# Performance work log

Hardware: AMD Instinct MI355X
Metric: run time of the kernel (lower is better)

## Reference

```python
import jax, jax.numpy as jnp
import numpy as np

N_NODES = 50000
N_EDGES = 800000


def gcn_conv(x, W, b, src, dst, n):
    """PyG-style GCNConv: add self-loops, symmetric deg normalization,
    out[i] = sum_{j->i} deg[i]^-1/2 deg[j]^-1/2 (x @ W)[j] + b."""
    h = x @ W                                   # [n, d_out]
    loop = jnp.arange(n, dtype=src.dtype)
    s = jnp.concatenate([src, loop])            # sources incl self-loops
    d = jnp.concatenate([dst, loop])            # destinations incl self-loops
    deg = jax.ops.segment_sum(jnp.ones_like(d, dtype=h.dtype), d, num_segments=n)
    dinv = jax.lax.rsqrt(jnp.maximum(deg, 1.0))
    norm = dinv[s] * dinv[d]                    # [E+n]
    msg = norm[:, None] * h[s]                  # gather + scale, [E+n, d_out]
    out = jax.ops.segment_sum(msg, d, num_segments=n)  # scatter-add
    return out + b


def setup_inputs() -> dict:
    key = jax.random.key(0)
    ks = jax.random.split(key, 8)
    x = jax.random.normal(ks[0], (N_NODES, 128), dtype=jnp.float32)
    edge_index = jax.random.randint(ks[1], (2, N_EDGES), 0, N_NODES, dtype=jnp.int64)
    def glorot(k, shape):
        lim = np.sqrt(6.0 / (shape[0] + shape[1])).astype(np.float32)
        return jax.random.uniform(k, shape, dtype=jnp.float32, minval=-lim, maxval=lim)
    return {
        "x": x,
        "edge_index": edge_index,
        "W1": glorot(ks[2], (128, 128)), "b1": jnp.zeros((128,), jnp.float32),
        "W2": glorot(ks[3], (128, 64)),  "b2": jnp.zeros((64,), jnp.float32),
        "W3": glorot(ks[4], (64, 16)),   "b3": jnp.zeros((16,), jnp.float32),
    }


def reference(x, edge_index, W1, b1, W2, b2, W3, b3):
    src, dst = edge_index[0], edge_index[1]
    n = x.shape[0]
    # base_model: 2-layer GCN
    h = gcn_conv(x, W1, b1, src, dst, n)
    h = jax.nn.relu(h)
    h = gcn_conv(h, W2, b2, src, dst, n)
    # added layer + softmax over class dim
    logits = gcn_conv(h, W3, b3, src, dst, n)
    return jax.nn.softmax(logits, axis=1)
```

## Files before the change

### kernel.cpp

```cpp
#include <hip/hip_runtime.h>
#include <hip/hip_fp16.h>

#define CAP 64


template<int DIN, int DOUT, int TM, int TN, int KC, int EPB>
__global__ __launch_bounds__(256) void k_fused1(const float* __restrict__ X,
                                                const float* __restrict__ W,
                                                __half* __restrict__ Y, int n, int G_scat,
                                                const int* __restrict__ src,
                                                const int* __restrict__ dst,
                                                int* __restrict__ cnt,
                                                unsigned short* __restrict__ srcS, int E) {
    constexpr int CG = DOUT / TN;
    constexpr int RG = 256 / CG;
    constexpr int TILE_R = RG * TM;
    constexpr int NCHUNK = DIN / KC;
    constexpr int XS = KC + 4;
    __shared__ float wsh[KC * DOUT];
    __shared__ float xs[TILE_R * XS];

    if (blockIdx.x < G_scat) {
        int base = blockIdx.x * 256 * EPB + threadIdx.x;
#pragma unroll
        for (int k = 0; k < EPB; ++k) {
            int e = base + k * 256;
            if (e < E) {
                int d = dst[e];
                int pos = atomicAdd(&cnt[d], 1);
                if (pos < CAP) srcS[(size_t)d * CAP + pos] = (unsigned short)src[e];
            }
        }
        return;
    }

    const int rb = (blockIdx.x - G_scat) * TILE_R;
    const int cg = threadIdx.x % CG;
    const int rg = threadIdx.x / CG;
    const int c0 = cg * TN;
    const int r0 = rg * TM;

    float acc[TM][TN] = {};

    for (int kc = 0; kc < NCHUNK; ++kc) {
        const int k0 = kc * KC;
        const float4* wg = reinterpret_cast<const float4*>(W + (size_t)k0 * DOUT);
        for (int i = threadIdx.x; i < KC * DOUT / 4; i += 256)
            reinterpret_cast<float4*>(wsh)[i] = wg[i];
        for (int i = threadIdx.x; i < TILE_R * KC / 4; i += 256) {
            int r = i / (KC / 4);
            int kk = (i % (KC / 4)) * 4;
            int row = rb + r;
            float4 v = {0.f, 0.f, 0.f, 0.f};
            if (row < n) v = *reinterpret_cast<const float4*>(X + (size_t)row * DIN + k0 + kk);
            *reinterpret_cast<float4*>(&xs[r * XS + kk]) = v;
        }
        __syncthreads();
#pragma unroll 4
        for (int k = 0; k < KC; ++k) {
            float wr[TN], xr[TM];
#pragma unroll
            for (int j = 0; j < TN; j += 4)
                *reinterpret_cast<float4*>(&wr[j]) =
                    *reinterpret_cast<const float4*>(&wsh[k * DOUT + c0 + j]);
#pragma unroll
            for (int i = 0; i < TM; ++i) xr[i] = xs[(r0 + i) * XS + k];
#pragma unroll
            for (int i = 0; i < TM; ++i)
#pragma unroll
                for (int j = 0; j < TN; ++j)
                    acc[i][j] = fmaf(xr[i], wr[j], acc[i][j]);
        }
        __syncthreads();
    }

#pragma unroll
    for (int i = 0; i < TM; ++i) {
        int row = rb + r0 + i;
        if (row < n) {
            union { float4 f4; __half h[8]; } u;
#pragma unroll
            for (int j = 0; j < TN; ++j) u.h[j] = __float2half_rn(acc[i][j]);
            *reinterpret_cast<float4*>(Y + (size_t)row * DOUT + c0) = u.f4;
        }
    }
}


__global__ __launch_bounds__(256) void k_g1_gemm2(const __half* __restrict__ t1,
                                                  const int* __restrict__ cnt,
                                                  const unsigned short* __restrict__ srcS,
                                                  const float* __restrict__ b1,
                                                  const float* __restrict__ W2,
                                                  __half* __restrict__ t2, int n) {
    __shared__ float h_sh[32][132];
    const int rb = blockIdx.x * 32;
    const int tid = threadIdx.x;
    const int c = tid & 15;
    const int gl = tid >> 4;

    for (int pass = 0; pass < 2; ++pass) {
        const int lrow = pass * 16 + gl;
        const int i = rb + lrow;
        if (i < n) {
            const int ci = cnt[i];
            const float di = rsqrtf((float)ci + 1.0f);
            float acc[8];
            float4 v = reinterpret_cast<const float4*>(t1)[(size_t)i * 16 + c];
            const __half2* hp = reinterpret_cast<const __half2*>(&v);
#pragma unroll
            for (int q = 0; q < 4; ++q) {
                float2 f = __half22float2(hp[q]);
                acc[2 * q] = di * f.x; acc[2 * q + 1] = di * f.y;
            }
            const int e1 = min(ci, CAP);
            const unsigned short* sp = srcS + (size_t)i * CAP;
#pragma unroll 4
            for (int e = 0; e < e1; ++e) {
                int s = sp[e];
                float ds = rsqrtf((float)cnt[s] + 1.0f);
                float4 w = reinterpret_cast<const float4*>(t1)[(size_t)s * 16 + c];
                const __half2* wp = reinterpret_cast<const __half2*>(&w);
#pragma unroll
                for (int q = 0; q < 4; ++q) {
                    float2 f = __half22float2(wp[q]);
                    acc[2 * q]     = fmaf(ds, f.x, acc[2 * q]);
                    acc[2 * q + 1] = fmaf(ds, f.y, acc[2 * q + 1]);
                }
            }
#pragma unroll
            for (int q = 0; q < 8; ++q) {
                float r = fmaf(di, acc[q], b1[c * 8 + q]);
                h_sh[lrow][c * 8 + q] = fmaxf(r, 0.f);
            }
        } else {
#pragma unroll
            for (int q = 0; q < 8; ++q) h_sh[lrow][c * 8 + q] = 0.f;
        }
    }
    __syncthreads();

    const int c0 = (tid & 15) * 4;
    const int r0 = (tid >> 4) * 2;
    float facc[2][4] = {};
#pragma unroll 8
    for (int k = 0; k < 128; ++k) {
        float4 wr = *reinterpret_cast<const float4*>(W2 + (size_t)k * 64 + c0);
        float x0 = h_sh[r0][k];
        float x1 = h_sh[r0 + 1][k];
        facc[0][0] = fmaf(x0, wr.x, facc[0][0]); facc[0][1] = fmaf(x0, wr.y, facc[0][1]);
        facc[0][2] = fmaf(x0, wr.z, facc[0][2]); facc[0][3] = fmaf(x0, wr.w, facc[0][3]);
        facc[1][0] = fmaf(x1, wr.x, facc[1][0]); facc[1][1] = fmaf(x1, wr.y, facc[1][1]);
        facc[1][2] = fmaf(x1, wr.z, facc[1][2]); facc[1][3] = fmaf(x1, wr.w, facc[1][3]);
    }
#pragma unroll
    for (int i = 0; i < 2; ++i) {
        int row = rb + r0 + i;
        if (row < n) {
            float di = rsqrtf((float)cnt[row] + 1.0f);
            union { float2 f2; __half h[4]; } u;
#pragma unroll
            for (int j = 0; j < 4; ++j) u.h[j] = __float2half_rn(di * facc[i][j]);
            *reinterpret_cast<float2*>(t2 + (size_t)row * 64 + c0) = u.f2;
        }
    }
}


__global__ __launch_bounds__(256) void k_g2_gemm3(const __half* __restrict__ t2,
                                                  const int* __restrict__ cnt,
                                                  const unsigned short* __restrict__ srcS,
                                                  const float* __restrict__ b2,
                                                  const float* __restrict__ W3,
                                                  __half* __restrict__ t3, int n) {
    __shared__ float h_sh[32][68];
    __shared__ float wsh[64 * 16];
    const int rb = blockIdx.x * 32;
    const int tid = threadIdx.x;
    const int c = tid & 7;
    const int g = tid >> 3;
    const int i = rb + g;
    if (i < n) {
        const int ci = cnt[i];
        const float di = rsqrtf((float)ci + 1.0f);
        float acc[8];
        float4 v = reinterpret_cast<const float4*>(t2)[(size_t)i * 8 + c];
        const __half2* hp = reinterpret_cast<const __half2*>(&v);
#pragma unroll
        for (int q = 0; q < 4; ++q) {
            float2 f = __half22float2(hp[q]);
            acc[2 * q] = f.x; acc[2 * q + 1] = f.y;
        }
        const int e1 = min(ci, CAP);
        const unsigned short* sp = srcS + (size_t)i * CAP;
#pragma unroll 4
        for (int e = 0; e < e1; ++e) {
            int s = sp[e];
            float4 w = reinterpret_cast<const float4*>(t2)[(size_t)s * 8 + c];
            const __half2* wp = reinterpret_cast<const __half2*>(&w);
#pragma unroll
            for (int q = 0; q < 4; ++q) {
                float2 f = __half22float2(wp[q]);
                acc[2 * q] += f.x; acc[2 * q + 1] += f.y;
            }
        }
#pragma unroll
        for (int q = 0; q < 8; ++q)
            h_sh[g][c * 8 + q] = fmaf(di, acc[q], b2[c * 8 + q]);
    } else {
#pragma unroll
        for (int q = 0; q < 8; ++q) h_sh[g][c * 8 + q] = 0.f;
    }
    __syncthreads();
    reinterpret_cast<float4*>(wsh)[tid] = reinterpret_cast<const float4*>(W3)[tid];
    __syncthreads();

    const int row = tid >> 3;
    const int col2 = (tid & 7) * 2;
    float a0 = 0.f, a1 = 0.f;
#pragma unroll 8
    for (int k = 0; k < 64; ++k) {
        float x = h_sh[row][k];
        a0 = fmaf(x, wsh[k * 16 + col2], a0);
        a1 = fmaf(x, wsh[k * 16 + col2 + 1], a1);
    }
    int grow = rb + row;
    if (grow < n) {
        float di = rsqrtf((float)cnt[grow] + 1.0f);
        union { unsigned int u32; __half h[2]; } u;
        u.h[0] = __float2half_rn(di * a0);
        u.h[1] = __float2half_rn(di * a1);
        *reinterpret_cast<unsigned int*>(t3 + (size_t)grow * 16 + col2) = u.u32;
    }
}


__global__ __launch_bounds__(256) void k_g3_softmax(const __half* __restrict__ t3,
                                                    const int* __restrict__ cnt,
                                                    const unsigned short* __restrict__ srcS,
                                                    const float* __restrict__ b3,
                                                    float* __restrict__ out, int n) {
    int tid = blockIdx.x * 256 + threadIdx.x;
    int i = tid >> 1;
    if (i >= n) return;
    int c = tid & 1;
    const float4* t4 = reinterpret_cast<const float4*>(t3);
    float acc[8];
    {
        float4 v = t4[(size_t)i * 2 + c];
        const __half2* hp = reinterpret_cast<const __half2*>(&v);
#pragma unroll
        for (int q = 0; q < 4; ++q) {
            float2 f = __half22float2(hp[q]);
            acc[2 * q] = f.x; acc[2 * q + 1] = f.y;
        }
    }
    const int ci = cnt[i];
    const float di = rsqrtf((float)ci + 1.0f);
    const int e1 = min(ci, CAP);
    const unsigned short* sp = srcS + (size_t)i * CAP;
#pragma unroll 4
    for (int e = 0; e < e1; ++e) {
        int s = sp[e];
        float4 v = t4[(size_t)s * 2 + c];
        const __half2* hp = reinterpret_cast<const __half2*>(&v);
#pragma unroll
        for (int q = 0; q < 4; ++q) {
            float2 f = __half22float2(hp[q]);
            acc[2 * q] += f.x; acc[2 * q + 1] += f.y;
        }
    }
    float r[8];
    const float* bp = b3 + c * 8;
#pragma unroll
    for (int q = 0; q < 8; ++q) r[q] = fmaf(di, acc[q], bp[q]);
    float m = r[0];
#pragma unroll
    for (int q = 1; q < 8; ++q) m = fmaxf(m, r[q]);
    m = fmaxf(m, __shfl_xor(m, 1, 2));
    float s = 0.f;
#pragma unroll
    for (int q = 0; q < 8; ++q) { r[q] = __expf(r[q] - m); s += r[q]; }
    s += __shfl_xor(s, 1, 2);
    float inv = 1.f / s;
    float4* o4 = reinterpret_cast<float4*>(out + ((size_t)i * 2 + c) * 8);
    float4 w0 = {r[0] * inv, r[1] * inv, r[2] * inv, r[3] * inv};
    float4 w1 = {r[4] * inv, r[5] * inv, r[6] * inv, r[7] * inv};
    o4[0] = w0; o4[1] = w1;
}


extern "C" void kernel_launch(void* const* d_in, const int* in_sizes, int n_in,
                              void* d_out, int out_size, void* d_ws, size_t ws_size,
                              hipStream_t stream) {
    const float* x  = (const float*)d_in[0];
    const int*   ei = (const int*)d_in[1];
    const float* W1 = (const float*)d_in[2];
    const float* b1 = (const float*)d_in[3];
    const float* W2 = (const float*)d_in[4];
    const float* b2 = (const float*)d_in[5];
    const float* W3 = (const float*)d_in[6];
    const float* b3 = (const float*)d_in[7];

    const int n = in_sizes[0] / 128;
    const int E = in_sizes[1] / 2;
    const int* srcp = ei;
    const int* dstp = ei + E;

    auto align = [](size_t v) { return (v + 255) & ~(size_t)255; };
    char* ws = (char*)d_ws;
    size_t o = 0;
    int*            cnt  = (int*)(ws + o);            o += align((size_t)n * 4);
    unsigned short* srcS = (unsigned short*)(ws + o); o += align((size_t)n * CAP * 2);
    __half*         t1   = (__half*)(ws + o);         o += align((size_t)n * 128 * 2);
    __half*         t2   = (__half*)(ws + o);         o += align((size_t)n * 64 * 2);
    __half*         t3   = (__half*)(ws + o);         o += align((size_t)n * 16 * 2);

    auto cdiv = [](long long a, long long b) { return (int)((a + b - 1) / b); };

    hipMemsetAsync(cnt, 0, (size_t)n * 4, stream);

    const int G_gemm = cdiv(n, 64);
    const int G_scat = cdiv(E, 256 * 2);
    k_fused1<128, 128, 4, 8, 16, 2><<<G_scat + G_gemm, 256, 0, stream>>>(
        x, W1, t1, n, G_scat, srcp, dstp, cnt, srcS, E);

    k_g1_gemm2<<<cdiv(n, 32), 256, 0, stream>>>(t1, cnt, srcS, b1, W2, t2, n);

    k_g2_gemm3<<<cdiv(n, 32), 256, 0, stream>>>(t2, cnt, srcS, b2, W3, t3, n);

    k_g3_softmax<<<cdiv((long long)n * 2, 256), 256, 0, stream>>>(
        t3, cnt, srcS, b3, (float*)d_out, n);
}
```

Before: 241.5 us.

## Prescale layer-1 features by inverse degree and cache dinv array

Adds a prescale kernel that computes the inverse square-root degree once per node, stores it in a dinv array, and multiplies t1 rows in place by it. The layer-1 gather loop can then drop its per-edge cnt[s] load and rsqrt. The later kernels read dinv instead of recomputing it. The change also reorders the fused kernel's blocks so GEMM blocks come before scatter blocks, and raises the K-chunk size from 16 to 32. In exchange there is an extra kernel launch and an extra read-write pass over t1, and t1 is rounded to half precision a second time.

After: 217.9 us. 1.11x faster.

```diff
diff --git a/kernel.cpp b/kernel.cpp
--- a/kernel.cpp
+++ b/kernel.cpp
@@ -7,7 +7,7 @@
 template<int DIN, int DOUT, int TM, int TN, int KC, int EPB>
 __global__ __launch_bounds__(256) void k_fused1(const float* __restrict__ X,
                                                 const float* __restrict__ W,
-                                                __half* __restrict__ Y, int n, int G_scat,
+                                                __half* __restrict__ Y, int n, int G_gemm,
                                                 const int* __restrict__ src,
                                                 const int* __restrict__ dst,
                                                 int* __restrict__ cnt,
@@ -20,8 +20,8 @@
     __shared__ float wsh[KC * DOUT];
     __shared__ float xs[TILE_R * XS];
 
-    if (blockIdx.x < G_scat) {
-        int base = blockIdx.x * 256 * EPB + threadIdx.x;
+    if (blockIdx.x >= G_gemm) {
+        int base = (blockIdx.x - G_gemm) * 256 * EPB + threadIdx.x;
 #pragma unroll
         for (int k = 0; k < EPB; ++k) {
             int e = base + k * 256;
@@ -34,7 +34,7 @@
         return;
     }
 
-    const int rb = (blockIdx.x - G_scat) * TILE_R;
+    const int rb = blockIdx.x * TILE_R;
     const int cg = threadIdx.x % CG;
     const int rg = threadIdx.x / CG;
     const int c0 = cg * TN;
@@ -87,8 +87,30 @@
 }
 
 
+__global__ __launch_bounds__(256) void k_prescale(const int* __restrict__ cnt,
+                                                  float* __restrict__ dinv,
+                                                  __half* __restrict__ t1, int n) {
+    int tid = blockIdx.x * 256 + threadIdx.x;
+    int i = tid >> 4;
+    if (i >= n) return;
+    int c = tid & 15;
+    float di = rsqrtf((float)cnt[i] + 1.0f);
+    if (c == 0) dinv[i] = di;
+    float4 v = reinterpret_cast<float4*>(t1)[(size_t)i * 16 + c];
+    __half2* h = reinterpret_cast<__half2*>(&v);
+#pragma unroll
+    for (int q = 0; q < 4; ++q) {
+        float2 f = __half22float2(h[q]);
+        f.x *= di; f.y *= di;
+        h[q] = __float22half2_rn(f);
+    }
+    reinterpret_cast<float4*>(t1)[(size_t)i * 16 + c] = v;
+}
+
+
 __global__ __launch_bounds__(256) void k_g1_gemm2(const __half* __restrict__ t1,
                                                   const int* __restrict__ cnt,
+                                                  const float* __restrict__ dinv,
                                                   const unsigned short* __restrict__ srcS,
                                                   const float* __restrict__ b1,
                                                   const float* __restrict__ W2,
@@ -103,29 +125,26 @@
         const int lrow = pass * 16 + gl;
         const int i = rb + lrow;
         if (i < n) {
-            const int ci = cnt[i];
-            const float di = rsqrtf((float)ci + 1.0f);
+            const float di = dinv[i];
             float acc[8];
             float4 v = reinterpret_cast<const float4*>(t1)[(size_t)i * 16 + c];
             const __half2* hp = reinterpret_cast<const __half2*>(&v);
 #pragma unroll
             for (int q = 0; q < 4; ++q) {
                 float2 f = __half22float2(hp[q]);
-                acc[2 * q] = di * f.x; acc[2 * q + 1] = di * f.y;
-            }
-            const int e1 = min(ci, CAP);
+                acc[2 * q] = f.x; acc[2 * q + 1] = f.y;
+            }
+            const int e1 = min(cnt[i], CAP);
             const unsigned short* sp = srcS + (size_t)i * CAP;
 #pragma unroll 4
             for (int e = 0; e < e1; ++e) {
                 int s = sp[e];
-                float ds = rsqrtf((float)cnt[s] + 1.0f);
                 float4 w = reinterpret_cast<const float4*>(t1)[(size_t)s * 16 + c];
                 const __half2* wp = reinterpret_cast<const __half2*>(&w);
 #pragma unroll
                 for (int q = 0; q < 4; ++q) {
                     float2 f = __half22float2(wp[q]);
-                    acc[2 * q]     = fmaf(ds, f.x, acc[2 * q]);
-                    acc[2 * q + 1] = fmaf(ds, f.y, acc[2 * q + 1]);
+                    acc[2 * q] += f.x; acc[2 * q + 1] += f.y;
                 }
             }
 #pragma unroll
@@ -157,7 +176,7 @@
     for (int i = 0; i < 2; ++i) {
         int row = rb + r0 + i;
         if (row < n) {
-            float di = rsqrtf((float)cnt[row] + 1.0f);
+            float di = dinv[row];
             union { float2 f2; __half h[4]; } u;
 #pragma unroll
             for (int j = 0; j < 4; ++j) u.h[j] = __float2half_rn(di * facc[i][j]);
@@ -169,6 +188,7 @@
 
 __global__ __launch_bounds__(256) void k_g2_gemm3(const __half* __restrict__ t2,
                                                   const int* __restrict__ cnt,
+                                                  const float* __restrict__ dinv,
                                                   const unsigned short* __restrict__ srcS,
                                                   const float* __restrict__ b2,
                                                   const float* __restrict__ W3,
@@ -181,8 +201,7 @@
     const int g = tid >> 3;
     const int i = rb + g;
     if (i < n) {
-        const int ci = cnt[i];
-        const float di = rsqrtf((float)ci + 1.0f);
+        const float di = dinv[i];
         float acc[8];
         float4 v = reinterpret_cast<const float4*>(t2)[(size_t)i * 8 + c];
         const __half2* hp = reinterpret_cast<const __half2*>(&v);
@@ -191,7 +210,7 @@
             float2 f = __half22float2(hp[q]);
             acc[2 * q] = f.x; acc[2 * q + 1] = f.y;
         }
-        const int e1 = min(ci, CAP);
+        const int e1 = min(cnt[i], CAP);
         const unsigned short* sp = srcS + (size_t)i * CAP;
 #pragma unroll 4
         for (int e = 0; e < e1; ++e) {
@@ -226,7 +245,7 @@
     }
     int grow = rb + row;
     if (grow < n) {
-        float di = rsqrtf((float)cnt[grow] + 1.0f);
+        float di = dinv[grow];
         union { unsigned int u32; __half h[2]; } u;
         u.h[0] = __float2half_rn(di * a0);
         u.h[1] = __float2half_rn(di * a1);
@@ -237,6 +256,7 @@
 
 __global__ __launch_bounds__(256) void k_g3_softmax(const __half* __restrict__ t3,
                                                     const int* __restrict__ cnt,
+                                                    const float* __restrict__ dinv,
                                                     const unsigned short* __restrict__ srcS,
                                                     const float* __restrict__ b3,
                                                     float* __restrict__ out, int n) {
@@ -255,9 +275,8 @@
             acc[2 * q] = f.x; acc[2 * q + 1] = f.y;
         }
     }
-    const int ci = cnt[i];
-    const float di = rsqrtf((float)ci + 1.0f);
-    const int e1 = min(ci, CAP);
+    const float di = dinv[i];
+    const int e1 = min(cnt[i], CAP);
     const unsigned short* sp = srcS + (size_t)i * CAP;
 #pragma unroll 4
     for (int e = 0; e < e1; ++e) {
@@ -311,6 +330,7 @@
     char* ws = (char*)d_ws;
     size_t o = 0;
     int*            cnt  = (int*)(ws + o);            o += align((size_t)n * 4);
+    float*          dinv = (float*)(ws + o);          o += align((size_t)n * 4);
     unsigned short* srcS = (unsigned short*)(ws + o); o += align((size_t)n * CAP * 2);
     __half*         t1   = (__half*)(ws + o);         o += align((size_t)n * 128 * 2);
     __half*         t2   = (__half*)(ws + o);         o += align((size_t)n * 64 * 2);
@@ -322,13 +342,15 @@
 
     const int G_gemm = cdiv(n, 64);
     const int G_scat = cdiv(E, 256 * 2);
-    k_fused1<128, 128, 4, 8, 16, 2><<<G_scat + G_gemm, 256, 0, stream>>>(
-        x, W1, t1, n, G_scat, srcp, dstp, cnt, srcS, E);
-
-    k_g1_gemm2<<<cdiv(n, 32), 256, 0, stream>>>(t1, cnt, srcS, b1, W2, t2, n);
-
-    k_g2_gemm3<<<cdiv(n, 32), 256, 0, stream>>>(t2, cnt, srcS, b2, W3, t3, n);
+    k_fused1<128, 128, 4, 8, 32, 2><<<G_gemm + G_scat, 256, 0, stream>>>(
+        x, W1, t1, n, G_gemm, srcp, dstp, cnt, srcS, E);
+
+    k_prescale<<<cdiv((long long)n * 16, 256), 256, 0, stream>>>(cnt, dinv, t1, n);
+
+    k_g1_gemm2<<<cdiv(n, 32), 256, 0, stream>>>(t1, cnt, dinv, srcS, b1, W2, t2, n);
+
+    k_g2_gemm3<<<cdiv(n, 32), 256, 0, stream>>>(t2, cnt, dinv, srcS, b2, W3, t3, n);
 
     k_g3_softmax<<<cdiv((long long)n * 2, 256), 256, 0, stream>>>(
-        t3, cnt, srcS, b3, (float*)d_out, n);
-}
+        t3, cnt, dinv, srcS, b3, (float*)d_out, n);
+}
```

## Split edge gathers across wave lanes with shuffle reduction; read W1 directly from global

Applied to the files above, without the earlier changes.

The gather stages of layers 1 and 2 now give each destination node a whole wavefront. The node's edges are split across lane groups and the partial sums are combined with xor shuffles, which raises memory-level parallelism for the irregular neighbor loads. The first GEMM stops staging W in shared memory and reads W rows straight from global/L1, uses KC=32, and places GEMM blocks before scatter blocks in the grid. The trade-offs are extra shuffle work, idle lanes on low-degree nodes, and possible extra global traffic for W.

After: 277.7 us. 1.15x slower.

```diff
diff --git a/kernel.cpp b/kernel.cpp
--- a/kernel.cpp
+++ b/kernel.cpp
@@ -7,7 +7,7 @@
 template<int DIN, int DOUT, int TM, int TN, int KC, int EPB>
 __global__ __launch_bounds__(256) void k_fused1(const float* __restrict__ X,
                                                 const float* __restrict__ W,
-                                                __half* __restrict__ Y, int n, int G_scat,
+                                                __half* __restrict__ Y, int n, int G_gemm,
                                                 const int* __restrict__ src,
                                                 const int* __restrict__ dst,
                                                 int* __restrict__ cnt,
@@ -17,11 +17,10 @@
     constexpr int TILE_R = RG * TM;
     constexpr int NCHUNK = DIN / KC;
     constexpr int XS = KC + 4;
-    __shared__ float wsh[KC * DOUT];
     __shared__ float xs[TILE_R * XS];
 
-    if (blockIdx.x < G_scat) {
-        int base = blockIdx.x * 256 * EPB + threadIdx.x;
+    if (blockIdx.x >= G_gemm) {
+        int base = (blockIdx.x - G_gemm) * 256 * EPB + threadIdx.x;
 #pragma unroll
         for (int k = 0; k < EPB; ++k) {
             int e = base + k * 256;
@@ -34,7 +33,7 @@
         return;
     }
 
-    const int rb = (blockIdx.x - G_scat) * TILE_R;
+    const int rb = blockIdx.x * TILE_R;
     const int cg = threadIdx.x % CG;
     const int rg = threadIdx.x / CG;
     const int c0 = cg * TN;
@@ -44,9 +43,6 @@
 
     for (int kc = 0; kc < NCHUNK; ++kc) {
         const int k0 = kc * KC;
-        const float4* wg = reinterpret_cast<const float4*>(W + (size_t)k0 * DOUT);
-        for (int i = threadIdx.x; i < KC * DOUT / 4; i += 256)
-            reinterpret_cast<float4*>(wsh)[i] = wg[i];
         for (int i = threadIdx.x; i < TILE_R * KC / 4; i += 256) {
             int r = i / (KC / 4);
             int kk = (i % (KC / 4)) * 4;
@@ -58,11 +54,10 @@
         __syncthreads();
 #pragma unroll 4
         for (int k = 0; k < KC; ++k) {
+            const float* wrow = W + (size_t)(k0 + k) * DOUT + c0;
             float wr[TN], xr[TM];
-#pragma unroll
-            for (int j = 0; j < TN; j += 4)
-                *reinterpret_cast<float4*>(&wr[j]) =
-                    *reinterpret_cast<const float4*>(&wsh[k * DOUT + c0 + j]);
+            *reinterpret_cast<float4*>(&wr[0]) = *reinterpret_cast<const float4*>(wrow);
+            *reinterpret_cast<float4*>(&wr[4]) = *reinterpret_cast<const float4*>(wrow + 4);
 #pragma unroll
             for (int i = 0; i < TM; ++i) xr[i] = xs[(r0 + i) * XS + k];
 #pragma unroll
@@ -96,27 +91,31 @@
     __shared__ float h_sh[32][132];
     const int rb = blockIdx.x * 32;
     const int tid = threadIdx.x;
-    const int c = tid & 15;
-    const int gl = tid >> 4;
-
-    for (int pass = 0; pass < 2; ++pass) {
-        const int lrow = pass * 16 + gl;
-        const int i = rb + lrow;
+    const int wave = tid >> 6;
+    const int lane = tid & 63;
+    const int c = lane & 15;
+    const int g = lane >> 4;
+
+    for (int nl = wave; nl < 32; nl += 4) {
+        const int i = rb + nl;
+        float acc[8] = {};
+        float di = 0.f;
         if (i < n) {
             const int ci = cnt[i];
-            const float di = rsqrtf((float)ci + 1.0f);
-            float acc[8];
-            float4 v = reinterpret_cast<const float4*>(t1)[(size_t)i * 16 + c];
-            const __half2* hp = reinterpret_cast<const __half2*>(&v);
-#pragma unroll
-            for (int q = 0; q < 4; ++q) {
-                float2 f = __half22float2(hp[q]);
-                acc[2 * q] = di * f.x; acc[2 * q + 1] = di * f.y;
+            di = rsqrtf((float)ci + 1.0f);
+            if (g == 0) {
+                float4 v = reinterpret_cast<const float4*>(t1)[(size_t)i * 16 + c];
+                const __half2* hp = reinterpret_cast<const __half2*>(&v);
+#pragma unroll
+                for (int q = 0; q < 4; ++q) {
+                    float2 f = __half22float2(hp[q]);
+                    acc[2 * q] = di * f.x; acc[2 * q + 1] = di * f.y;
+                }
             }
             const int e1 = min(ci, CAP);
             const unsigned short* sp = srcS + (size_t)i * CAP;
-#pragma unroll 4
-            for (int e = 0; e < e1; ++e) {
+#pragma unroll 2
+            for (int e = g; e < e1; e += 4) {
                 int s = sp[e];
                 float ds = rsqrtf((float)cnt[s] + 1.0f);
                 float4 w = reinterpret_cast<const float4*>(t1)[(size_t)s * 16 + c];
@@ -128,14 +127,20 @@
                     acc[2 * q + 1] = fmaf(ds, f.y, acc[2 * q + 1]);
                 }
             }
+        }
+#pragma unroll
+        for (int q = 0; q < 8; ++q) {
+            float v = acc[q];
+            v += __shfl_xor(v, 16);
+            v += __shfl_xor(v, 32);
+            acc[q] = v;
+        }
+        if (g == 0) {
 #pragma unroll
             for (int q = 0; q < 8; ++q) {
-                float r = fmaf(di, acc[q], b1[c * 8 + q]);
-                h_sh[lrow][c * 8 + q] = fmaxf(r, 0.f);
-            }
-        } else {
-#pragma unroll
-            for (int q = 0; q < 8; ++q) h_sh[lrow][c * 8 + q] = 0.f;
+                float r = (i < n) ? fmaxf(fmaf(di, acc[q], b1[c * 8 + q]), 0.f) : 0.f;
+                h_sh[nl][c * 8 + q] = r;
+            }
         }
     }
     __syncthreads();
@@ -177,39 +182,53 @@
     __shared__ float wsh[64 * 16];
     const int rb = blockIdx.x * 32;
     const int tid = threadIdx.x;
-    const int c = tid & 7;
-    const int g = tid >> 3;
-    const int i = rb + g;
-    if (i < n) {
-        const int ci = cnt[i];
-        const float di = rsqrtf((float)ci + 1.0f);
-        float acc[8];
-        float4 v = reinterpret_cast<const float4*>(t2)[(size_t)i * 8 + c];
-        const __half2* hp = reinterpret_cast<const __half2*>(&v);
-#pragma unroll
-        for (int q = 0; q < 4; ++q) {
-            float2 f = __half22float2(hp[q]);
-            acc[2 * q] = f.x; acc[2 * q + 1] = f.y;
-        }
-        const int e1 = min(ci, CAP);
-        const unsigned short* sp = srcS + (size_t)i * CAP;
-#pragma unroll 4
-        for (int e = 0; e < e1; ++e) {
-            int s = sp[e];
-            float4 w = reinterpret_cast<const float4*>(t2)[(size_t)s * 8 + c];
-            const __half2* wp = reinterpret_cast<const __half2*>(&w);
-#pragma unroll
-            for (int q = 0; q < 4; ++q) {
-                float2 f = __half22float2(wp[q]);
-                acc[2 * q] += f.x; acc[2 * q + 1] += f.y;
-            }
-        }
-#pragma unroll
-        for (int q = 0; q < 8; ++q)
-            h_sh[g][c * 8 + q] = fmaf(di, acc[q], b2[c * 8 + q]);
-    } else {
-#pragma unroll
-        for (int q = 0; q < 8; ++q) h_sh[g][c * 8 + q] = 0.f;
+    const int wave = tid >> 6;
+    const int lane = tid & 63;
+    const int c = lane & 7;
+    const int g = lane >> 3;
+
+    for (int nl = wave; nl < 32; nl += 4) {
+        const int i = rb + nl;
+        float acc[8] = {};
+        float di = 0.f;
+        if (i < n) {
+            const int ci = cnt[i];
+            di = rsqrtf((float)ci + 1.0f);
+            if (g == 0) {
+                float4 v = reinterpret_cast<const float4*>(t2)[(size_t)i * 8 + c];
+                const __half2* hp = reinterpret_cast<const __half2*>(&v);
+#pragma unroll
+                for (int q = 0; q < 4; ++q) {
+                    float2 f = __half22float2(hp[q]);
+                    acc[2 * q] = f.x; acc[2 * q + 1] = f.y;
+                }
+            }
+            const int e1 = min(ci, CAP);
+            const unsigned short* sp = srcS + (size_t)i * CAP;
+            for (int e = g; e < e1; e += 8) {
+                int s = sp[e];
+                float4 w = reinterpret_cast<const float4*>(t2)[(size_t)s * 8 + c];
+                const __half2* wp = reinterpret_cast<const __half2*>(&w);
+#pragma unroll
+                for (int q = 0; q < 4; ++q) {
+                    float2 f = __half22float2(wp[q]);
+                    acc[2 * q] += f.x; acc[2 * q + 1] += f.y;
+                }
+            }
+        }
+#pragma unroll
+        for (int q = 0; q < 8; ++q) {
+            float v = acc[q];
+            v += __shfl_xor(v, 8);
+            v += __shfl_xor(v, 16);
+            v += __shfl_xor(v, 32);
+            acc[q] = v;
+        }
+        if (g == 0) {
+#pragma unroll
+            for (int q = 0; q < 8; ++q)
+                h_sh[nl][c * 8 + q] = (i < n) ? fmaf(di, acc[q], b2[c * 8 + q]) : 0.f;
+        }
     }
     __syncthreads();
     reinterpret_cast<float4*>(wsh)[tid] = reinterpret_cast<const float4*>(W3)[tid];
@@ -322,8 +341,8 @@
 
     const int G_gemm = cdiv(n, 64);
     const int G_scat = cdiv(E, 256 * 2);
-    k_fused1<128, 128, 4, 8, 16, 2><<<G_scat + G_gemm, 256, 0, stream>>>(
-        x, W1, t1, n, G_scat, srcp, dstp, cnt, srcS, E);
+    k_fused1<128, 128, 4, 8, 32, 2><<<G_gemm + G_scat, 256, 0, stream>>>(
+        x, W1, t1, n, G_gemm, srcp, dstp, cnt, srcS, E);
 
     k_g1_gemm2<<<cdiv(n, 32), 256, 0, stream>>>(t1, cnt, srcS, b1, W2, t2, n);
 
```
